# Kernel optimization log

Hardware: AMD Instinct MI355X
Metric: run time of the kernel (lower is better)

The kernel has to match this reference:

```python
import jax, jax.numpy as jnp
import numpy as np

TEMPERATURE = 0.1
KNN = 5
NEG = -1e30   # finite stand-in for -inf: identical softmax/threshold result, NaN-safe
EPS = -1e-08  # note: the original code really adds a NEGATIVE epsilon
MASK_VAL = -1.0


def setup_inputs() -> dict:
    key = jax.random.key(0)
    k1, k2, k3, k4 = jax.random.split(key, 4)
    n_img, max_r, n_cap, max_w, d = 128, 36, 128, 32, 512
    imgs = jax.random.normal(k1, (n_img, max_r, d), dtype=jnp.float32)
    caps = jax.random.normal(k2, (n_cap, max_w, d), dtype=jnp.float32)
    img_lens = jax.random.randint(k3, (n_img,), KNN + 1, max_r + 1, dtype=jnp.int32)
    cap_lens = jax.random.randint(k4, (n_cap,), 4, max_w + 1, dtype=jnp.int32)
    # guarantee lens.max() equals the static dims (torch slices to lens.max())
    img_lens = img_lens.at[0].set(max_r)
    cap_lens = cap_lens.at[0].set(max_w)
    return {"imgs": imgs, "caps": caps, "img_lens": img_lens, "cap_lens": cap_lens}


def reference(imgs, caps, img_lens, cap_lens):
    n_img, max_r, d = imgs.shape
    n_cap, max_w, _ = caps.shape
    knn = min(KNN, max_r)

    img_valid = jnp.arange(max_r)[None, :] < img_lens[:, None]   # [n_img, max_r]
    cap_valid = jnp.arange(max_w)[None, :] < cap_lens[:, None]   # [n_cap, max_w]
    imgs = jnp.where(img_valid[..., None], imgs, 0.0)
    caps = jnp.where(cap_valid[..., None], caps, 0.0)

    # fine-grained all-pairs similarities: [n_cap, n_img, max_w, max_r]
    sims = jnp.einsum('cwd,ird->ciwr', caps, imgs) / TEMPERATURE
    mask = cap_valid[:, None, :, None] & img_valid[None, :, None, :]
    sims = jnp.where(mask, sims, NEG)

    # top-KNN threshold along region axis (== sort()[..., max_r-KNN] in torch)
    kth = jax.lax.top_k(sims, knn)[0][..., -1:]
    sims = jnp.where(sims < kth, NEG, sims)

    attn = jax.nn.softmax(sims, axis=-1)
    attn = jnp.where(mask, attn, 0.0)

    att = jnp.einsum('ciwr,ird->ciwd', attn, imgs)                # attended regions
    num = jnp.einsum('ciwd,cwd->ciw', att, caps)
    den = jnp.linalg.norm(att, axis=-1) + EPS
    out = num / den                                               # [n_cap, n_img, max_w]
    out = jnp.where(cap_valid[:, None, :], out, MASK_VAL)
    return jnp.transpose(out, (1, 0, 2))                          # [n_img, n_cap, max_w]
```

## Files before the change

### kernel.cpp

```cpp
#include <hip/hip_runtime.h>
#include <cmath>

#define N_IMG 128
#define MAX_R 36
#define N_CAP 128
#define MAX_W 32
#define DIM   512
#define NEGV  -1e30f

typedef unsigned short u16;
typedef unsigned int   u32;
typedef unsigned char  u8;
typedef __attribute__((ext_vector_type(4))) int i32x4;

#define NI_ELEMS (N_IMG * MAX_R * DIM)
#define NC_ELEMS (N_CAP * MAX_W * DIM)

#define A_CHUNK 18432
#define B_CHUNK 16384
#define BUF_BYTES 34816
#define LDS_BYTES 69632

__device__ __forceinline__ void gload_lds16(const void* g, void* l) {
    __builtin_amdgcn_global_load_lds(
        (const __attribute__((address_space(1))) void*)g,
        (__attribute__((address_space(3))) void*)l, 16, 0, 0);
}

__global__ __launch_bounds__(256) void convert_kernel(const float* __restrict__ imgs,
                                                      const float* __restrict__ caps,
                                                      u8* __restrict__ imgsT,
                                                      u8* __restrict__ capsT) {
    const size_t ni4 = NI_ELEMS / 4;
    const size_t total4 = (NI_ELEMS + NC_ELEMS) / 4;
    const size_t stride = (size_t)gridDim.x * blockDim.x;
    for (size_t p = (size_t)blockIdx.x * blockDim.x + threadIdx.x; p < total4; p += stride) {
        const bool isImg = p < ni4;
        const float4 v = isImg ? ((const float4*)imgs)[p] : ((const float4*)caps)[p - ni4];
        const int q0 = (int)rintf(fminf(fmaxf(v.x * 4096.f, -32639.f), 32639.f));
        const int q1 = (int)rintf(fminf(fmaxf(v.y * 4096.f, -32639.f), 32639.f));
        const int q2 = (int)rintf(fminf(fmaxf(v.z * 4096.f, -32639.f), 32639.f));
        const int q3 = (int)rintf(fminf(fmaxf(v.w * 4096.f, -32639.f), 32639.f));
        const int h0 = (q0 + 128) >> 8, l0 = q0 - (h0 << 8);
        const int h1 = (q1 + 128) >> 8, l1 = q1 - (h1 << 8);
        const int h2 = (q2 + 128) >> 8, l2 = q2 - (h2 << 8);
        const int h3 = (q3 + 128) >> 8, l3 = q3 - (h3 << 8);
        const u32 hw = (u32)(h0 & 255) | ((u32)(h1 & 255) << 8) |
                       ((u32)(h2 & 255) << 16) | ((u32)(h3 & 255) << 24);
        const u32 lw = (u32)(l0 & 255) | ((u32)(l1 & 255) << 8) |
                       ((u32)(l2 & 255) << 16) | ((u32)(l3 & 255) << 24);
        if (isImg) {
            const int e = (int)(p * 4);
            const int imgRow = e >> 9, k = e & 511;
            const int g = imgRow / 144;
            const int rowT = imgRow - g * 144;
            const int kb = k >> 6, k6 = k & 63;
            const int blk = (k6 >> 4) ^ ((rowT >> 1) & 3);
            const size_t off = (size_t)(g * 8 + kb) * A_CHUNK + rowT * 64 + blk * 16 + (k6 & 15);
            *(u32*)(imgsT + off) = hw;
            *(u32*)(imgsT + off + 9216) = lw;
        } else {
            const int e = (int)((p - ni4) * 4);
            const int R = e >> 9, k = e & 511;
            const int cg = R >> 7, row = R & 127;
            const int kb = k >> 6, k6 = k & 63;
            const int blk = (k6 >> 4) ^ ((row >> 1) & 3);
            const size_t off = (size_t)(cg * 8 + kb) * B_CHUNK + row * 64 + blk * 16 + (k6 & 15);
            *(u32*)(capsT + off) = hw;
            *(u32*)(capsT + off + 8192) = lw;
        }
    }
}

__global__ __launch_bounds__(256) void gram_kernel(const float* __restrict__ imgs,
                                                   float* __restrict__ G) {
    const int i = blockIdx.x;
    const int t = threadIdx.x;
    __shared__ float sImg[MAX_R][132];
    const float* base = imgs + (size_t)i * MAX_R * DIM;

    const int ap = t / 12;
    const int bt = t % 12;
    const bool active = ap < 18;
    float acc[2][3] = {};

    for (int ch = 0; ch < 4; ++ch) {
        for (int idx = t; idx < MAX_R * 32; idx += 256) {
            const int row = idx >> 5, col = idx & 31;
            *(float4*)&sImg[row][col * 4] =
                *(const float4*)(base + row * DIM + ch * 128 + col * 4);
        }
        __syncthreads();
        if (active) {
            #pragma unroll
            for (int k4 = 0; k4 < 32; ++k4) {
                float4 a0 = *(float4*)&sImg[ap * 2 + 0][k4 * 4];
                float4 a1 = *(float4*)&sImg[ap * 2 + 1][k4 * 4];
                float4 b0 = *(float4*)&sImg[bt * 3 + 0][k4 * 4];
                float4 b1 = *(float4*)&sImg[bt * 3 + 1][k4 * 4];
                float4 b2 = *(float4*)&sImg[bt * 3 + 2][k4 * 4];
                acc[0][0] += a0.x*b0.x + a0.y*b0.y + a0.z*b0.z + a0.w*b0.w;
                acc[0][1] += a0.x*b1.x + a0.y*b1.y + a0.z*b1.z + a0.w*b1.w;
                acc[0][2] += a0.x*b2.x + a0.y*b2.y + a0.z*b2.z + a0.w*b2.w;
                acc[1][0] += a1.x*b0.x + a1.y*b0.y + a1.z*b0.z + a1.w*b0.w;
                acc[1][1] += a1.x*b1.x + a1.y*b1.y + a1.z*b1.z + a1.w*b1.w;
                acc[1][2] += a1.x*b2.x + a1.y*b2.y + a1.z*b2.z + a1.w*b2.w;
            }
        }
        __syncthreads();
    }
    if (active) {
        float* g = G + (size_t)i * (MAX_R * MAX_R);
        #pragma unroll
        for (int x = 0; x < 2; ++x)
            #pragma unroll
            for (int y = 0; y < 3; ++y)
                g[(ap * 2 + x) * MAX_R + (bt * 3 + y)] = acc[x][y];
    }
}

__global__ __launch_bounds__(256, 2) void vsc_mfma_kernel(const u8* __restrict__ imgsT,
                                const u8* __restrict__ capsT,
                                const int* __restrict__ img_lens,
                                const int* __restrict__ cap_lens,
                                const float* __restrict__ G,
                                float* __restrict__ out) {
    extern __shared__ __align__(16) char smem[];
    const int bid = blockIdx.x;
    const int xcd = bid & 7;
    const int r_  = bid >> 3;
    const int g   = (r_ >> 5) * 8 + xcd;
    const int cg  = r_ & 31;
    const int t = threadIdx.x;
    const int wid = t >> 6;
    const int lane = t & 63;
    const int l15 = lane & 15;
    const int kblk = lane >> 4;

    const u8* gA = imgsT + (size_t)g * 8 * A_CHUNK;
    const u8* gB = capsT + (size_t)cg * 8 * B_CHUNK;

    auto stage = [&](int kb, char* buf) {
        if (wid < 2) {
            const u8* src = gA + (size_t)kb * A_CHUNK + wid * 9216 + lane * 16;
            char* dst = buf + wid * 9216;
            #pragma unroll
            for (int jj = 0; jj < 9; ++jj)
                gload_lds16(src + jj * 1024, dst + jj * 1024);
        } else {
            const int wb = wid - 2;
            const u8* src = gB + (size_t)kb * B_CHUNK + wb * 8192 + lane * 16;
            char* dst = buf + 18432 + wb * 8192;
            #pragma unroll
            for (int jj = 0; jj < 8; ++jj)
                gload_lds16(src + jj * 1024, dst + jj * 1024);
        }
    };

    i32x4 accH[9][2], accC[9][2];
    #pragma unroll
    for (int mt = 0; mt < 9; ++mt)
        #pragma unroll
        for (int nt = 0; nt < 2; ++nt) {
            accH[mt][nt] = (i32x4){0, 0, 0, 0};
            accC[mt][nt] = (i32x4){0, 0, 0, 0};
        }

    stage(0, smem);
    __syncthreads();

    const int blk16 = (kblk ^ ((l15 >> 1) & 3)) << 4;
    const int baseA = l15 * 64 + blk16;
    const int baseB = (wid * 32 + l15) * 64 + blk16;

    for (int kb = 0; kb < 8; ++kb) {
        char* cur = smem + (size_t)(kb & 1) * BUF_BYTES;
        if (kb < 7) stage(kb + 1, smem + (size_t)((kb + 1) & 1) * BUF_BYTES);

        const i32x4 bh0 = *(const i32x4*)(cur + 18432 + baseB);
        const i32x4 bl0 = *(const i32x4*)(cur + 26624 + baseB);
        const i32x4 bh1 = *(const i32x4*)(cur + 18432 + baseB + 1024);
        const i32x4 bl1 = *(const i32x4*)(cur + 26624 + baseB + 1024);
        #pragma unroll
        for (int mt = 0; mt < 9; ++mt) {
            const i32x4 ah = *(const i32x4*)(cur + baseA + mt * 1024);
            const i32x4 al = *(const i32x4*)(cur + 9216 + baseA + mt * 1024);
            accH[mt][0] = __builtin_amdgcn_mfma_i32_16x16x64_i8(ah, bh0, accH[mt][0], 0, 0, 0);
            accH[mt][1] = __builtin_amdgcn_mfma_i32_16x16x64_i8(ah, bh1, accH[mt][1], 0, 0, 0);
            accC[mt][0] = __builtin_amdgcn_mfma_i32_16x16x64_i8(ah, bl0, accC[mt][0], 0, 0, 0);
            accC[mt][0] = __builtin_amdgcn_mfma_i32_16x16x64_i8(al, bh0, accC[mt][0], 0, 0, 0);
            accC[mt][1] = __builtin_amdgcn_mfma_i32_16x16x64_i8(ah, bl1, accC[mt][1], 0, 0, 0);
            accC[mt][1] = __builtin_amdgcn_mfma_i32_16x16x64_i8(al, bh1, accC[mt][1], 0, 0, 0);
            i32x4 lt0 = (i32x4){0, 0, 0, 0};
            i32x4 lt1 = (i32x4){0, 0, 0, 0};
            lt0 = __builtin_amdgcn_mfma_i32_16x16x64_i8(al, bl0, lt0, 0, 0, 0);
            lt1 = __builtin_amdgcn_mfma_i32_16x16x64_i8(al, bl1, lt1, 0, 0, 0);
            #pragma unroll
            for (int e = 0; e < 4; ++e) {
                accC[mt][0][e] += (lt0[e] + 128) >> 8;
                accC[mt][1][e] += (lt1[e] + 128) >> 8;
            }
        }
        __syncthreads();
    }

    float* sG = (float*)smem;
    {
        const float4* src = (const float4*)(G + (size_t)g * 4 * 1296);
        for (int idx = t; idx < 1296; idx += 256)
            ((float4*)sG)[idx] = src[idx];
    }
    __syncthreads();

    int ilen_[4];
    #pragma unroll
    for (int j = 0; j < 4; ++j) ilen_[j] = img_lens[g * 4 + j];

    #pragma unroll
    for (int nt = 0; nt < 2; ++nt) {
        const int col = wid * 32 + nt * 16 + l15;
        const int c = cg * 4 + (col >> 5);
        const int w = col & 31;
        const int clen = cap_lens[c];
        #pragma unroll
        for (int j = 0; j < 4; ++j) {
            const int mtb = (36 * j) >> 4;
            const int ilenj = ilen_[j];
            float tv0 = NEGV, tv1 = NEGV, tv2 = NEGV, tv3 = NEGV, tv4 = NEGV;
            #pragma unroll
            for (int dm = 0; dm < 3; ++dm) {
                #pragma unroll
                for (int e = 0; e < 4; ++e) {
                    const int mt = mtb + dm;
                    const int r = mt * 16 + kblk * 4 + e;
                    const int rr = r - 36 * j;
                    const float sval = (float)accH[mt][nt][e] * (10.f / 256.f)
                                     + (float)accC[mt][nt][e] * (10.f / 65536.f);
                    float v = NEGV;
                    if ((unsigned)rr < (unsigned)ilenj)
                        v = __uint_as_float((__float_as_uint(sval) & ~63u) | (u32)rr);
                    const bool c0 = v > tv0, c1 = v > tv1, c2 = v > tv2, c3 = v > tv3, c4 = v > tv4;
                    const float n4 = c4 ? (c3 ? tv3 : v) : tv4;
                    const float n3 = c3 ? (c2 ? tv2 : v) : tv3;
                    const float n2 = c2 ? (c1 ? tv1 : v) : tv2;
                    const float n1 = c1 ? (c0 ? tv0 : v) : tv1;
                    const float n0 = c0 ? v : tv0;
                    tv0 = n0; tv1 = n1; tv2 = n2; tv3 = n3; tv4 = n4;
                }
            }
            float ta[5] = {tv0, tv1, tv2, tv3, tv4};
            #pragma unroll
            for (int st = 0; st < 2; ++st) {
                const int dx = 16 << st;
                float tb[5];
                #pragma unroll
                for (int s = 0; s < 5; ++s) tb[s] = __shfl_xor(ta[s], dx);
                float na[5];
                #pragma unroll
                for (int k = 0; k < 5; ++k) {
                    float best = fmaxf(ta[k], tb[k]);
                    #pragma unroll
                    for (int i2 = 1; i2 <= k; ++i2)
                        best = fmaxf(best, fminf(ta[i2 - 1], tb[k - i2]));
                    na[k] = best;
                }
                #pragma unroll
                for (int s = 0; s < 5; ++s) ta[s] = na[s];
            }
            const float m = ta[0];
            const float p0 = 1.f;
            const float p1 = expf(ta[1] - m);
            const float p2 = expf(ta[2] - m);
            const float p3 = expf(ta[3] - m);
            const float p4 = expf(ta[4] - m);
            const float sum = p0 + p1 + p2 + p3 + p4;
            const float num = p0 * ta[0] + p1 * ta[1] + p2 * ta[2] + p3 * ta[3] + p4 * ta[4];
            const int r0 = __float_as_uint(ta[0]) & 63;
            const int r1 = __float_as_uint(ta[1]) & 63;
            const int r2 = __float_as_uint(ta[2]) & 63;
            const int r3 = __float_as_uint(ta[3]) & 63;
            const int r4 = __float_as_uint(ta[4]) & 63;
            const float* gj = sG + j * 1296;
            const float pa = (kblk == 0) ? p0 : (kblk == 1) ? p1 : (kblk == 2) ? p2 : p3;
            const int   ra = (kblk == 0) ? r0 : (kblk == 1) ? r1 : (kblk == 2) ? r2 : r3;
            const float* grow = gj + ra * 36;
            float part = pa * (p0 * grow[r0] + p1 * grow[r1] + p2 * grow[r2]
                             + p3 * grow[r3] + p4 * grow[r4]);
            if (kblk == 0) {
                const float* grow4 = gj + r4 * 36;
                part += p4 * (p0 * grow4[r0] + p1 * grow4[r1] + p2 * grow4[r2]
                            + p3 * grow4[r3] + p4 * grow4[r4]);
            }
            part += __shfl_xor(part, 16);
            part += __shfl_xor(part, 32);
            if (kblk == j) {
                float result = -1.f;
                if (w < clen) {
                    const float inv = 1.f / sum;
                    const float a_ = 0.1f * num * inv;
                    const float den = sqrtf(part) * inv + (-1e-8f);
                    result = a_ / den;
                }
                out[((size_t)(g * 4 + j) * N_CAP + c) * MAX_W + w] = result;
            }
        }
    }
}

extern "C" void kernel_launch(void* const* d_in, const int* in_sizes, int n_in,
                              void* d_out, int out_size, void* d_ws, size_t ws_size,
                              hipStream_t stream) {
    const float* imgs     = (const float*)d_in[0];
    const float* caps     = (const float*)d_in[1];
    const int*   img_lens = (const int*)d_in[2];
    const int*   cap_lens = (const int*)d_in[3];
    float* out = (float*)d_out;

    float* G  = (float*)d_ws;
    u8* imgsT = (u8*)d_ws + 663552;
    u8* capsT = imgsT + (size_t)32 * 8 * A_CHUNK;

    hipFuncSetAttribute((const void*)vsc_mfma_kernel,
                        hipFuncAttributeMaxDynamicSharedMemorySize, LDS_BYTES);

    convert_kernel<<<2048, 256, 0, stream>>>(imgs, caps, imgsT, capsT);
    gram_kernel<<<N_IMG, 256, 0, stream>>>(imgs, G);
    vsc_mfma_kernel<<<1024, 256, LDS_BYTES, stream>>>(imgsT, capsT, img_lens, cap_lens, G, out);
}
```

Measured before the change: 94.33 us.

## Compute image Gram matrix with int8 MFMA from pre-split tensors; tweak main loop

Measured after the change: 78.70 us. 1.2x faster.

```diff
diff --git a/kernel.cpp b/kernel.cpp
--- a/kernel.cpp
+++ b/kernel.cpp
@@ -72,50 +72,86 @@
     }
 }
 
-__global__ __launch_bounds__(256) void gram_kernel(const float* __restrict__ imgs,
-                                                   float* __restrict__ G) {
-    const int i = blockIdx.x;
+__global__ __launch_bounds__(256) void gram_i8_kernel(const u8* __restrict__ imgsT,
+                                                      float* __restrict__ G) {
+    const int i  = blockIdx.x;
+    const int gg = i >> 2;
+    const int m  = i & 3;
     const int t = threadIdx.x;
-    __shared__ float sImg[MAX_R][132];
-    const float* base = imgs + (size_t)i * MAX_R * DIM;
-
-    const int ap = t / 12;
-    const int bt = t % 12;
-    const bool active = ap < 18;
-    float acc[2][3] = {};
-
-    for (int ch = 0; ch < 4; ++ch) {
-        for (int idx = t; idx < MAX_R * 32; idx += 256) {
-            const int row = idx >> 5, col = idx & 31;
-            *(float4*)&sImg[row][col * 4] =
-                *(const float4*)(base + row * DIM + ch * 128 + col * 4);
+    const int wid = t >> 6;
+    const int lane = t & 63;
+    const int l15 = lane & 15;
+    const int kq = lane >> 4;
+
+    __shared__ __align__(16) u8 sT[2][2][3072];
+
+    const u8* base = imgsT + (size_t)gg * 8 * A_CHUNK + m * 36 * 64;
+
+    auto stage = [&](int kb, int buf) {
+        const u8* hsrc = base + (size_t)kb * A_CHUNK;
+        {
+            const int u = t;
+            if (u < 144) gload_lds16(hsrc + u * 16, &sT[buf][0][u * 16]);
+            else if (u < 288) gload_lds16(hsrc + 9216 + (u - 144) * 16, &sT[buf][1][(u - 144) * 16]);
+        }
+        if (t < 32) {
+            const int u = 112 + t;
+            gload_lds16(hsrc + 9216 + u * 16, &sT[buf][1][u * 16]);
+        }
+    };
+
+    i32x4 aH[3], aC[3], aL[3];
+    #pragma unroll
+    for (int mt = 0; mt < 3; ++mt) {
+        aH[mt] = (i32x4){0,0,0,0};
+        aC[mt] = (i32x4){0,0,0,0};
+        aL[mt] = (i32x4){0,0,0,0};
+    }
+
+    stage(0, 0);
+    __syncthreads();
+
+    const int m18 = 18 * m;
+    for (int kb = 0; kb < 8; ++kb) {
+        const int buf = kb & 1;
+        if (kb < 7) stage(kb + 1, buf ^ 1);
+        if (wid < 3) {
+            const int brow = wid * 16 + l15;
+            const int bblk = kq ^ ((m18 + (brow >> 1)) & 3);
+            const i32x4 bh = *(const i32x4*)&sT[buf][0][brow * 64 + bblk * 16];
+            const i32x4 bl = *(const i32x4*)&sT[buf][1][brow * 64 + bblk * 16];
+            #pragma unroll
+            for (int mt = 0; mt < 3; ++mt) {
+                const int arow = mt * 16 + l15;
+                const int ablk = kq ^ ((m18 + (arow >> 1)) & 3);
+                const i32x4 ah = *(const i32x4*)&sT[buf][0][arow * 64 + ablk * 16];
+                const i32x4 al = *(const i32x4*)&sT[buf][1][arow * 64 + ablk * 16];
+                aH[mt] = __builtin_amdgcn_mfma_i32_16x16x64_i8(ah, bh, aH[mt], 0, 0, 0);
+                aC[mt] = __builtin_amdgcn_mfma_i32_16x16x64_i8(ah, bl, aC[mt], 0, 0, 0);
+                aC[mt] = __builtin_amdgcn_mfma_i32_16x16x64_i8(al, bh, aC[mt], 0, 0, 0);
+                aL[mt] = __builtin_amdgcn_mfma_i32_16x16x64_i8(al, bl, aL[mt], 0, 0, 0);
+            }
         }
         __syncthreads();
-        if (active) {
-            #pragma unroll
-            for (int k4 = 0; k4 < 32; ++k4) {
-                float4 a0 = *(float4*)&sImg[ap * 2 + 0][k4 * 4];
-                float4 a1 = *(float4*)&sImg[ap * 2 + 1][k4 * 4];
-                float4 b0 = *(float4*)&sImg[bt * 3 + 0][k4 * 4];
-                float4 b1 = *(float4*)&sImg[bt * 3 + 1][k4 * 4];
-                float4 b2 = *(float4*)&sImg[bt * 3 + 2][k4 * 4];
-                acc[0][0] += a0.x*b0.x + a0.y*b0.y + a0.z*b0.z + a0.w*b0.w;
-                acc[0][1] += a0.x*b1.x + a0.y*b1.y + a0.z*b1.z + a0.w*b1.w;
-                acc[0][2] += a0.x*b2.x + a0.y*b2.y + a0.z*b2.z + a0.w*b2.w;
-                acc[1][0] += a1.x*b0.x + a1.y*b0.y + a1.z*b0.z + a1.w*b0.w;
-                acc[1][1] += a1.x*b1.x + a1.y*b1.y + a1.z*b1.z + a1.w*b1.w;
-                acc[1][2] += a1.x*b2.x + a1.y*b2.y + a1.z*b2.z + a1.w*b2.w;
-            }
-        }
-        __syncthreads();
-    }
-    if (active) {
-        float* g = G + (size_t)i * (MAX_R * MAX_R);
-        #pragma unroll
-        for (int x = 0; x < 2; ++x)
-            #pragma unroll
-            for (int y = 0; y < 3; ++y)
-                g[(ap * 2 + x) * MAX_R + (bt * 3 + y)] = acc[x][y];
+    }
+
+    if (wid < 3) {
+        const int col = wid * 16 + l15;
+        if (col < 36) {
+            #pragma unroll
+            for (int mt = 0; mt < 3; ++mt) {
+                #pragma unroll
+                for (int e = 0; e < 4; ++e) {
+                    const int row = mt * 16 + kq * 4 + e;
+                    if (row < 36) {
+                        const float g = (float)aH[mt][e] * (1.f / 256.f)
+                                      + (float)aC[mt][e] * (1.f / 65536.f)
+                                      + (float)aL[mt][e] * (1.f / 16777216.f);
+                        G[(size_t)i * 1296 + row * 36 + col] = g;
+                    }
+                }
+            }
+        }
     }
 }
 
@@ -181,26 +217,28 @@
         const i32x4 bl0 = *(const i32x4*)(cur + 26624 + baseB);
         const i32x4 bh1 = *(const i32x4*)(cur + 18432 + baseB + 1024);
         const i32x4 bl1 = *(const i32x4*)(cur + 26624 + baseB + 1024);
+        __builtin_amdgcn_s_setprio(1);
         #pragma unroll
         for (int mt = 0; mt < 9; ++mt) {
             const i32x4 ah = *(const i32x4*)(cur + baseA + mt * 1024);
             const i32x4 al = *(const i32x4*)(cur + 9216 + baseA + mt * 1024);
+            i32x4 lt0 = (i32x4){0, 0, 0, 0};
+            i32x4 lt1 = (i32x4){0, 0, 0, 0};
+            lt0 = __builtin_amdgcn_mfma_i32_16x16x64_i8(al, bl0, lt0, 0, 0, 0);
+            lt1 = __builtin_amdgcn_mfma_i32_16x16x64_i8(al, bl1, lt1, 0, 0, 0);
             accH[mt][0] = __builtin_amdgcn_mfma_i32_16x16x64_i8(ah, bh0, accH[mt][0], 0, 0, 0);
             accH[mt][1] = __builtin_amdgcn_mfma_i32_16x16x64_i8(ah, bh1, accH[mt][1], 0, 0, 0);
             accC[mt][0] = __builtin_amdgcn_mfma_i32_16x16x64_i8(ah, bl0, accC[mt][0], 0, 0, 0);
             accC[mt][0] = __builtin_amdgcn_mfma_i32_16x16x64_i8(al, bh0, accC[mt][0], 0, 0, 0);
             accC[mt][1] = __builtin_amdgcn_mfma_i32_16x16x64_i8(ah, bl1, accC[mt][1], 0, 0, 0);
             accC[mt][1] = __builtin_amdgcn_mfma_i32_16x16x64_i8(al, bh1, accC[mt][1], 0, 0, 0);
-            i32x4 lt0 = (i32x4){0, 0, 0, 0};
-            i32x4 lt1 = (i32x4){0, 0, 0, 0};
-            lt0 = __builtin_amdgcn_mfma_i32_16x16x64_i8(al, bl0, lt0, 0, 0, 0);
-            lt1 = __builtin_amdgcn_mfma_i32_16x16x64_i8(al, bl1, lt1, 0, 0, 0);
             #pragma unroll
             for (int e = 0; e < 4; ++e) {
-                accC[mt][0][e] += (lt0[e] + 128) >> 8;
-                accC[mt][1][e] += (lt1[e] + 128) >> 8;
-            }
-        }
+                accC[mt][0][e] += lt0[e] >> 8;
+                accC[mt][1][e] += lt1[e] >> 8;
+            }
+        }
+        __builtin_amdgcn_s_setprio(0);
         __syncthreads();
     }
 
@@ -324,6 +362,6 @@
                         hipFuncAttributeMaxDynamicSharedMemorySize, LDS_BYTES);
 
     convert_kernel<<<2048, 256, 0, stream>>>(imgs, caps, imgsT, capsT);
-    gram_kernel<<<N_IMG, 256, 0, stream>>>(imgs, G);
+    gram_i8_kernel<<<N_IMG, 256, 0, stream>>>(imgsT, G);
     vsc_mfma_kernel<<<1024, 256, LDS_BYTES, stream>>>(imgsT, capsT, img_lens, cap_lens, G, out);
 }
```
